# Optimization experiments

Measured on AMD Instinct MI355X. Metric: run time of the kernel, lower is better.

## Reference

```python
import jax, jax.numpy as jnp
import numpy as np

B, H, K, V = 64, 32, 128, 128


def setup_inputs() -> dict:
    key = jax.random.key(0)
    ks = jax.random.split(key, 7)
    q = jax.random.normal(ks[0], (B, 1, H, K), dtype=jnp.float32)
    k = jax.random.normal(ks[1], (B, 1, H, K), dtype=jnp.float32)
    v = jax.random.normal(ks[2], (B, 1, H, V), dtype=jnp.float32)
    # a = -kappa, b = kappa*a_gate in RWKV-7; plain gaussians suffice for a math reference
    a = jax.random.normal(ks[3], (B, 1, H, K), dtype=jnp.float32)
    b = jax.random.normal(ks[4], (B, 1, H, K), dtype=jnp.float32)
    # gk is a log-decay: negative so exp(gk) in (0, 1]
    gk = -jnp.abs(jax.random.normal(ks[5], (B, 1, H, K), dtype=jnp.float32)) * 0.1
    h0 = jax.random.normal(ks[6], (B, H, K, V), dtype=jnp.float32) * 0.1
    return {"q": q, "k": k, "v": v, "a": a, "b": b, "gk": gk, "h0": h0}


def reference(q, k, v, a, b, gk, h0):
    """RWKV-7 DPLR single-step (T=1) decode recurrence, per (batch, head):
      g     = exp(gk)                                # [K] decay
      s     = a^T H0                                 # [V]
      t     = (q*g)^T H0                             # [V]
      alpha = q . b ; beta = q . k                   # scalars
      o     = t + alpha*s + beta*v                   # [V]
      Ht    = diag(g) H0 + b s^T + k v^T             # [K,V]
    Mirrors dplr_decode_t1_kernel_streamK exactly (fp32 accumulation).
    """
    qf = q[:, 0].astype(jnp.float32)   # [B,H,K]
    kf = k[:, 0].astype(jnp.float32)
    af = a[:, 0].astype(jnp.float32)
    bf = b[:, 0].astype(jnp.float32)
    vf = v[:, 0].astype(jnp.float32)   # [B,H,V]
    g = jnp.exp(gk[:, 0].astype(jnp.float32))  # [B,H,K]
    hf = h0.astype(jnp.float32)        # [B,H,K,V]

    s = jnp.einsum('bhk,bhkv->bhv', af, hf)
    t = jnp.einsum('bhk,bhkv->bhv', qf * g, hf)
    alpha = jnp.sum(qf * bf, axis=-1, keepdims=True)  # [B,H,1]
    beta = jnp.sum(qf * kf, axis=-1, keepdims=True)   # [B,H,1]
    o = t + alpha * s + beta * vf                      # [B,H,V]

    ht = g[..., None] * hf + bf[..., None] * s[:, :, None, :] + kf[..., None] * vf[:, :, None, :]
    return o[:, None].astype(v.dtype), ht.astype(h0.dtype)
```

## Files before the change

kernel.cpp:

```cpp
#include <hip/hip_runtime.h>


#define KD 128
#define VD 128
#define BH_TOTAL 2048

__global__ __launch_bounds__(256) void dplr_decode_t1_kernel(
    const float* __restrict__ q_,  const float* __restrict__ k_,
    const float* __restrict__ v_,  const float* __restrict__ a_,
    const float* __restrict__ b_,  const float* __restrict__ gk_,
    const float* __restrict__ h0_, float* __restrict__ out_)
{
    const int bh  = blockIdx.x;
    const int tid = threadIdx.x;
    const int c4  = (tid & 31) * 4;
    const int grp = tid >> 5;
    const int r0  = grp * 16;

    const size_t vec_off = (size_t)bh * KD;
    const size_t h_off   = (size_t)bh * (KD * VD);

    __shared__ float qs[KD], ks[KD], bs[KD], as_[KD], gs[KD], qgs[KD];
    __shared__ float sred[8][VD];
    __shared__ float tred[8][VD];
    __shared__ float scomb[VD];
    __shared__ float red2[2];

    float4 Hreg[16];
    const float* hp = h0_ + h_off + (size_t)r0 * VD + c4;
#pragma unroll
    for (int j = 0; j < 16; ++j) {
        Hreg[j] = *(const float4*)(hp + (size_t)j * VD);
    }

    const float4 v4 = *(const float4*)(v_ + vec_off + c4);

    if (tid < KD) {
        float qq = q_[vec_off + tid];
        float gg = expf(gk_[vec_off + tid]);
        qs[tid]  = qq;
        ks[tid]  = k_[vec_off + tid];
        bs[tid]  = b_[vec_off + tid];
        as_[tid] = a_[vec_off + tid];
        gs[tid]  = gg;
        qgs[tid] = qq * gg;
    }
    __syncthreads();

    if (tid < 64) {
        float p = qs[tid] * bs[tid] + qs[tid + 64] * bs[tid + 64];
#pragma unroll
        for (int o = 32; o > 0; o >>= 1) p += __shfl_down(p, o, 64);
        if (tid == 0) red2[0] = p;
    } else if (tid < 128) {
        int l = tid - 64;
        float p = qs[l] * ks[l] + qs[l + 64] * ks[l + 64];
#pragma unroll
        for (int o = 32; o > 0; o >>= 1) p += __shfl_down(p, o, 64);
        if (l == 0) red2[1] = p;
    }

    float4 sp = make_float4(0.f, 0.f, 0.f, 0.f);
    float4 tp = make_float4(0.f, 0.f, 0.f, 0.f);
#pragma unroll
    for (int j = 0; j < 16; ++j) {
        const float av = as_[r0 + j];
        const float qg = qgs[r0 + j];
        const float4 h = Hreg[j];
        sp.x += av * h.x; sp.y += av * h.y; sp.z += av * h.z; sp.w += av * h.w;
        tp.x += qg * h.x; tp.y += qg * h.y; tp.z += qg * h.z; tp.w += qg * h.w;
    }
    *(float4*)&sred[grp][c4] = sp;
    *(float4*)&tred[grp][c4] = tp;
    __syncthreads();

    if (tid < VD) {
        float sc = 0.f, tc = 0.f;
#pragma unroll
        for (int g = 0; g < 8; ++g) { sc += sred[g][tid]; tc += tred[g][tid]; }
        scomb[tid] = sc;
        const float vv = v_[vec_off + tid];
        out_[(size_t)bh * VD + tid] = tc + red2[0] * sc + red2[1] * vv;
    }
    __syncthreads();

    const float4 s4 = *(const float4*)&scomb[c4];
    float* op = out_ + (size_t)BH_TOTAL * VD + h_off + (size_t)r0 * VD + c4;
#pragma unroll
    for (int j = 0; j < 16; ++j) {
        const int r = r0 + j;
        const float gr = gs[r];
        const float br = bs[r];
        const float kr = ks[r];
        const float4 h = Hreg[j];
        float4 o4;
        o4.x = gr * h.x + br * s4.x + kr * v4.x;
        o4.y = gr * h.y + br * s4.y + kr * v4.y;
        o4.z = gr * h.z + br * s4.z + kr * v4.z;
        o4.w = gr * h.w + br * s4.w + kr * v4.w;
        *(float4*)(op + (size_t)j * VD) = o4;
    }
}

extern "C" void kernel_launch(void* const* d_in, const int* in_sizes, int n_in,
                              void* d_out, int out_size, void* d_ws, size_t ws_size,
                              hipStream_t stream) {
    const float* q  = (const float*)d_in[0];
    const float* k  = (const float*)d_in[1];
    const float* v  = (const float*)d_in[2];
    const float* a  = (const float*)d_in[3];
    const float* b  = (const float*)d_in[4];
    const float* gk = (const float*)d_in[5];
    const float* h0 = (const float*)d_in[6];
    float* out = (float*)d_out;

    dplr_decode_t1_kernel<<<BH_TOTAL, 256, 0, stream>>>(q, k, v, a, b, gk, h0, out);
}
```

Before: 250.2 us.

## Split each head's V columns across two blocks and reduce with wavefront shuffles

Each (batch, head) is now handled by two blocks, each owning 64 of the 128 V columns. That halves the per-thread H register tile from 16 to 8 float4s and doubles the grid, which should raise occupancy and memory-level parallelism for this bandwidth-bound state update. The cross-row partial sums for s and t are now combined within each wavefront by xor shuffles before a smaller shared-memory reduction. In exchange, both blocks reload the small q/k/a/b/gk vectors and recompute the alpha/beta dot products, and expf is swapped for the faster, less precise __expf.

Result: no change. 250.6 us (+0.1%).

```diff
diff --git a/kernel.cpp b/kernel.cpp
--- a/kernel.cpp
+++ b/kernel.cpp
@@ -5,41 +5,42 @@
 #define VD 128
 #define BH_TOTAL 2048
 
-__global__ __launch_bounds__(256) void dplr_decode_t1_kernel(
+__global__ __launch_bounds__(256, 4) void dplr_decode_t1_kernel(
     const float* __restrict__ q_,  const float* __restrict__ k_,
     const float* __restrict__ v_,  const float* __restrict__ a_,
     const float* __restrict__ b_,  const float* __restrict__ gk_,
     const float* __restrict__ h0_, float* __restrict__ out_)
 {
-    const int bh  = blockIdx.x;
-    const int tid = threadIdx.x;
-    const int c4  = (tid & 31) * 4;
-    const int grp = tid >> 5;
-    const int r0  = grp * 16;
+    const int bh   = blockIdx.x >> 1;
+    const int cb   = (blockIdx.x & 1) * 64;
+    const int tid  = threadIdx.x;
+    const int c    = (tid & 15) * 4;
+    const int col  = cb + c;
+    const int grp  = tid >> 4;
+    const int r0   = grp * 8;
+    const int wv   = tid >> 6;
 
     const size_t vec_off = (size_t)bh * KD;
     const size_t h_off   = (size_t)bh * (KD * VD);
 
-    __shared__ float qs[KD], ks[KD], bs[KD], as_[KD], gs[KD], qgs[KD];
-    __shared__ float sred[8][VD];
-    __shared__ float tred[8][VD];
-    __shared__ float scomb[VD];
+    __shared__ float qs[KD], ks_[KD], bs[KD], as_[KD], gs[KD], qgs[KD];
+    __shared__ float sred[4][64];
+    __shared__ float tred[4][64];
+    __shared__ float scomb[64];
     __shared__ float red2[2];
 
-    float4 Hreg[16];
-    const float* hp = h0_ + h_off + (size_t)r0 * VD + c4;
+    float4 Hreg[8];
+    const float* hp = h0_ + h_off + (size_t)r0 * VD + col;
 #pragma unroll
-    for (int j = 0; j < 16; ++j) {
+    for (int j = 0; j < 8; ++j)
         Hreg[j] = *(const float4*)(hp + (size_t)j * VD);
-    }
-
-    const float4 v4 = *(const float4*)(v_ + vec_off + c4);
+    const float4 v4 = *(const float4*)(v_ + vec_off + col);
 
     if (tid < KD) {
         float qq = q_[vec_off + tid];
-        float gg = expf(gk_[vec_off + tid]);
+        float gg = __expf(gk_[vec_off + tid]);
         qs[tid]  = qq;
-        ks[tid]  = k_[vec_off + tid];
+        ks_[tid] = k_[vec_off + tid];
         bs[tid]  = b_[vec_off + tid];
         as_[tid] = a_[vec_off + tid];
         gs[tid]  = gg;
@@ -54,7 +55,7 @@
         if (tid == 0) red2[0] = p;
     } else if (tid < 128) {
         int l = tid - 64;
-        float p = qs[l] * ks[l] + qs[l + 64] * ks[l + 64];
+        float p = qs[l] * ks_[l] + qs[l + 64] * ks_[l + 64];
 #pragma unroll
         for (int o = 32; o > 0; o >>= 1) p += __shfl_down(p, o, 64);
         if (l == 0) red2[1] = p;
@@ -63,35 +64,44 @@
     float4 sp = make_float4(0.f, 0.f, 0.f, 0.f);
     float4 tp = make_float4(0.f, 0.f, 0.f, 0.f);
 #pragma unroll
-    for (int j = 0; j < 16; ++j) {
+    for (int j = 0; j < 8; ++j) {
         const float av = as_[r0 + j];
         const float qg = qgs[r0 + j];
         const float4 h = Hreg[j];
         sp.x += av * h.x; sp.y += av * h.y; sp.z += av * h.z; sp.w += av * h.w;
         tp.x += qg * h.x; tp.y += qg * h.y; tp.z += qg * h.z; tp.w += qg * h.w;
     }
-    *(float4*)&sred[grp][c4] = sp;
-    *(float4*)&tred[grp][c4] = tp;
-    __syncthreads();
 
-    if (tid < VD) {
-        float sc = 0.f, tc = 0.f;
 #pragma unroll
-        for (int g = 0; g < 8; ++g) { sc += sred[g][tid]; tc += tred[g][tid]; }
-        scomb[tid] = sc;
-        const float vv = v_[vec_off + tid];
-        out_[(size_t)bh * VD + tid] = tc + red2[0] * sc + red2[1] * vv;
+    for (int o = 16; o <= 32; o <<= 1) {
+        sp.x += __shfl_xor(sp.x, o, 64); sp.y += __shfl_xor(sp.y, o, 64);
+        sp.z += __shfl_xor(sp.z, o, 64); sp.w += __shfl_xor(sp.w, o, 64);
+        tp.x += __shfl_xor(tp.x, o, 64); tp.y += __shfl_xor(tp.y, o, 64);
+        tp.z += __shfl_xor(tp.z, o, 64); tp.w += __shfl_xor(tp.w, o, 64);
+    }
+    if ((tid & 63) < 16) {
+        *(float4*)&sred[wv][c] = sp;
+        *(float4*)&tred[wv][c] = tp;
     }
     __syncthreads();
 
-    const float4 s4 = *(const float4*)&scomb[c4];
-    float* op = out_ + (size_t)BH_TOTAL * VD + h_off + (size_t)r0 * VD + c4;
+    if (tid < 64) {
+        float sc = sred[0][tid] + sred[1][tid] + sred[2][tid] + sred[3][tid];
+        float tc = tred[0][tid] + tred[1][tid] + tred[2][tid] + tred[3][tid];
+        scomb[tid] = sc;
+        const float vv = v_[vec_off + cb + tid];
+        out_[(size_t)bh * VD + cb + tid] = tc + red2[0] * sc + red2[1] * vv;
+    }
+    __syncthreads();
+
+    const float4 s4 = *(const float4*)&scomb[c];
+    float* op = out_ + (size_t)BH_TOTAL * VD + h_off + (size_t)r0 * VD + col;
 #pragma unroll
-    for (int j = 0; j < 16; ++j) {
+    for (int j = 0; j < 8; ++j) {
         const int r = r0 + j;
         const float gr = gs[r];
         const float br = bs[r];
-        const float kr = ks[r];
+        const float kr = ks_[r];
         const float4 h = Hreg[j];
         float4 o4;
         o4.x = gr * h.x + br * s4.x + kr * v4.x;
@@ -114,5 +124,5 @@
     const float* h0 = (const float*)d_in[6];
     float* out = (float*)d_out;
 
-    dplr_decode_t1_kernel<<<BH_TOTAL, 256, 0, stream>>>(q, k, v, a, b, gk, h0, out);
+    dplr_decode_t1_kernel<<<BH_TOTAL * 2, 256, 0, stream>>>(q, k, v, a, b, gk, h0, out);
 }
```
